# Performance work log

Hardware: AMD Instinct MI355X
Metric: run time of the kernel (lower is better)

Reference implementation:

```python
import jax, jax.numpy as jnp
import numpy as np

WINDOW_SIZE = 2
SOFTMAX_TEMP = 0.01


def get_indices(batch_size, window_size):
    # For each window, match keypoints of frame j against dense map of frame j+1.
    kp_inds, dense_inds = [], []
    for i in range(batch_size):
        for j in range(window_size - 1):
            idx = i * window_size + j
            kp_inds.append(idx)
            dense_inds.append(idx + 1)
    return np.array(kp_inds), np.array(dense_inds)


def l2_normalize(x, axis):
    n = jnp.sqrt(jnp.sum(x * x, axis=axis, keepdims=True))
    return x / jnp.maximum(n, 1e-12)


def grid_sample_bilinear(img, grid_u, grid_v):
    """torch.nn.functional.grid_sample, mode='bilinear', padding='zeros', align_corners=False.
    img: (B,C,H,W); grid_u, grid_v: (B,N) normalized coords in [-1,1]. Returns (B,C,N)."""
    B, C, H, W = img.shape
    x = ((grid_u + 1.0) * W - 1.0) * 0.5  # pixel x
    y = ((grid_v + 1.0) * H - 1.0) * 0.5  # pixel y
    x0 = jnp.floor(x)
    y0 = jnp.floor(y)
    wx1 = x - x0
    wy1 = y - y0
    flat = img.reshape(B, C, H * W)

    def gather(xi, yi):
        valid = (xi >= 0) & (xi <= W - 1) & (yi >= 0) & (yi <= H - 1)
        xi_c = jnp.clip(xi, 0, W - 1).astype(jnp.int32)
        yi_c = jnp.clip(yi, 0, H - 1).astype(jnp.int32)
        idx = yi_c * W + xi_c  # (B,N)
        vals = jnp.take_along_axis(flat, idx[:, None, :], axis=2)  # (B,C,N)
        return vals * valid[:, None, :].astype(img.dtype)

    out = (gather(x0, y0) * ((1 - wx1) * (1 - wy1))[:, None, :]
           + gather(x0 + 1, y0) * (wx1 * (1 - wy1))[:, None, :]
           + gather(x0, y0 + 1) * ((1 - wx1) * wy1)[:, None, :]
           + gather(x0 + 1, y0 + 1) * (wx1 * wy1)[:, None, :])
    return out


def setup_inputs() -> dict:
    key = jax.random.key(0)
    k1, k2, k3, k4 = jax.random.split(key, 4)
    BW, C, N, H, W = 8, 128, 512, 256, 256
    return {
        "keypoint_scores": jax.random.uniform(k1, (BW, 1, N), dtype=jnp.float32),
        "keypoint_desc": jax.random.normal(k2, (BW, C, N), dtype=jnp.float32),
        "scores_dense": jax.random.uniform(k3, (BW, 1, H, W), dtype=jnp.float32),
        "desc_dense": jax.random.normal(k4, (BW, C, H, W), dtype=jnp.float32),
    }


def reference(keypoint_scores, keypoint_desc, scores_dense, desc_dense):
    BW, C, N = keypoint_desc.shape
    batch_size = BW // WINDOW_SIZE
    _, _, H, W = desc_dense.shape
    kp_inds, dense_inds = get_indices(batch_size, WINDOW_SIZE)

    src_desc = l2_normalize(keypoint_desc[kp_inds], axis=1)  # (B,C,N)
    B = src_desc.shape[0]
    tgt_desc_dense = desc_dense[dense_inds]  # (B,C,H,W)
    tgt_unrolled = l2_normalize(tgt_desc_dense.reshape(B, C, H * W), axis=1)

    # cosine similarity scores (B,N,H*W) -> temperature softmax over dense map
    match_vals = jnp.einsum('bcn,bcm->bnm', src_desc, tgt_unrolled)
    soft_match_vals = jax.nn.softmax(match_vals / SOFTMAX_TEMP, axis=2)

    # soft-argmax: expected (u,v) pixel coordinates
    v_coord, u_coord = jnp.meshgrid(jnp.arange(H), jnp.arange(W), indexing='ij')
    coords = jnp.stack([u_coord.reshape(-1), v_coord.reshape(-1)], axis=1).astype(jnp.float32)  # (HW,2)
    pseudo_coords = jnp.einsum('bnm,mk->bnk', soft_match_vals, coords)  # (B,N,2)

    u_norm = 2.0 * pseudo_coords[:, :, 0] / (W - 1) - 1.0
    v_norm = 2.0 * pseudo_coords[:, :, 1] / (H - 1) - 1.0

    tgt_scores_dense = scores_dense[dense_inds]
    pseudo_scores = grid_sample_bilinear(tgt_scores_dense, u_norm, v_norm)  # (B,1,N)
    pseudo_desc = grid_sample_bilinear(tgt_desc_dense, u_norm, v_norm)      # (B,C,N)

    desc_match_score = jnp.sum(src_desc * pseudo_desc, axis=1, keepdims=True) / float(C)
    src_scores = keypoint_scores[kp_inds]
    match_weights = 0.5 * (desc_match_score + 1.0) * src_scores * pseudo_scores
    return (pseudo_coords, match_weights, soft_match_vals)
```

## Files before the change

### kernel.cpp

```cpp
#include <hip/hip_runtime.h>


typedef short  v8s __attribute__((ext_vector_type(8)));
typedef unsigned short v8u __attribute__((ext_vector_type(8)));
typedef float  v4f __attribute__((ext_vector_type(4)));

#define EXP2_SCALE 144.269504088896f
#define WAITV(N) asm volatile("s_waitcnt vmcnt(" #N ")" ::: "memory")
#define SBAR()   __builtin_amdgcn_s_barrier()
#define SCHED()  __builtin_amdgcn_sched_barrier(0)
#define PRIO(N)  __builtin_amdgcn_s_setprio(N)

static const size_t O_AHI  = 0;
static const size_t O_ALO  = O_AHI  + 262144ull*2;
static const size_t O_SRCN = O_ALO  + 262144ull*2;
static const size_t O_BHI  = O_SRCN + 262144ull*4;
static const size_t O_BLO  = O_BHI  + 33554432ull*2;
static const size_t O_PART = O_BLO  + 33554432ull*2;
static const size_t O_ROWS = O_PART + 2048ull*64*16;

static __device__ inline unsigned short f2bf(float x) {
    unsigned u = __float_as_uint(x);
    u = u + 0x7FFFu + ((u >> 16) & 1u);
    return (unsigned short)(u >> 16);
}
static __device__ inline float bf2f(unsigned short h) {
    return __uint_as_float(((unsigned)h) << 16);
}

__device__ __forceinline__ void gl_lds16(const void* g, void* l) {
    auto gp = (const __attribute__((address_space(1))) unsigned int*)(uintptr_t)g;
    auto lp = (__attribute__((address_space(3))) unsigned int*)(uintptr_t)l;
    __builtin_amdgcn_global_load_lds(gp, lp, 16, 0, 0);
}

__global__ void __launch_bounds__(256) k_prep_src(const float* __restrict__ kd,
                                                  float* __restrict__ srcN,
                                                  unsigned short* __restrict__ Ahi,
                                                  unsigned short* __restrict__ Alo) {
    int gw = blockIdx.x * 4 + (threadIdx.x >> 6);
    int l  = threadIdx.x & 63;
    int b  = gw >> 9, n = gw & 511;
    const float* base = kd + (size_t)(2 * b) * 128 * 512;
    float x0 = base[l * 512 + n];
    float x1 = base[(l + 64) * 512 + n];
    float ss = x0 * x0 + x1 * x1;
#pragma unroll
    for (int m = 1; m < 64; m <<= 1) ss += __shfl_xor(ss, m, 64);
    float inv = 1.0f / fmaxf(sqrtf(ss), 1e-12f);
    float xn0 = x0 * inv, xn1 = x1 * inv;
    int ob = gw * 128;
    srcN[ob + l] = xn0;  srcN[ob + l + 64] = xn1;
    unsigned short h0 = f2bf(xn0), h1 = f2bf(xn1);
    Ahi[ob + l] = h0;        Ahi[ob + l + 64] = h1;
    Alo[ob + l] = f2bf(xn0 - bf2f(h0));
    Alo[ob + l + 64] = f2bf(xn1 - bf2f(h1));
}

__global__ void __launch_bounds__(256) k_prep_tgt(const float* __restrict__ dd,
                                                  unsigned short* __restrict__ Bhi,
                                                  unsigned short* __restrict__ Blo) {
    int t = blockIdx.x * 128 + (threadIdx.x >> 1);
    int h = threadIdx.x & 1;
    int b = t >> 16;
    int p = t & 65535;
    const float* src = dd + (size_t)(2 * b + 1) * 128 * 65536 + (size_t)(h * 64) * 65536 + p;
    float v[64];
    float ss = 0.f;
#pragma unroll
    for (int c = 0; c < 64; ++c) { float x = src[(size_t)c * 65536]; v[c] = x; ss += x * x; }
    ss += __shfl_xor(ss, 1, 64);
    float inv = 1.0f / fmaxf(sqrtf(ss), 1e-12f);
    size_t ob = (size_t)t * 128 + h * 64;
#pragma unroll
    for (int c8 = 0; c8 < 8; ++c8) {
        v8u h8, l8;
#pragma unroll
        for (int j = 0; j < 8; ++j) {
            float xn = v[c8 * 8 + j] * inv;
            unsigned short hh = f2bf(xn);
            h8[j] = hh;
            l8[j] = f2bf(xn - bf2f(hh));
        }
        *(v8u*)(Bhi + ob + c8 * 8) = h8;
        *(v8u*)(Blo + ob + c8 * 8) = l8;
    }
}

template <int MODE>
__global__ void __launch_bounds__(512, 2) k_gemm(const unsigned short* __restrict__ Ahi,
                                                 const unsigned short* __restrict__ Alo,
                                                 const unsigned short* __restrict__ Bhi,
                                                 const unsigned short* __restrict__ Blo,
                                                 const float4* __restrict__ rows,
                                                 float* __restrict__ part,
                                                 float* __restrict__ out,
                                                 const float* __restrict__ ksc,
                                                 const float* __restrict__ sd,
                                                 const float* __restrict__ dd,
                                                 const float* __restrict__ srcN) {
    __shared__ v4f bstage4[8192];
    char* bstage = (char*)bstage4;

    const int tid = threadIdx.x;
    const int l = tid & 63, w = tid >> 6;
    const int wm = w >> 2, wn = w & 3;
    const int l15 = l & 15, l16 = l >> 4;
    const int mtg = blockIdx.x, ny = blockIdx.y, b = blockIdx.z;
    const int mt0 = mtg * 16;
    float* osm = out + 6144;

    v8s ahi[2][4], alo[2][4];
    {
        const size_t ar = ((size_t)(b * 512 + ny * 128 + wn * 32 + l15)) * 128 + l16 * 8;
#pragma unroll
        for (int nf = 0; nf < 2; ++nf)
#pragma unroll
            for (int ksl = 0; ksl < 4; ++ksl) {
                ahi[nf][ksl] = *(const v8s*)(Ahi + ar + nf * 2048 + ksl * 32);
                alo[nf][ksl] = *(const v8s*)(Alo + ar + nf * 2048 + ksl * 32);
            }
    }
    float invs[2];
    if (MODE == 1) {
#pragma unroll
        for (int nf = 0; nf < 2; ++nf)
            invs[nf] = rows[b * 512 + ny * 128 + wn * 32 + nf * 16 + l15].x;
    }
    WAITV(0);

    const size_t pxbase = ((size_t)b * 65536 + (size_t)mt0 * 128) * 128;

#define STAGEU(SRC, eoff, bufidx)                                                   \
    {                                                                               \
        const unsigned short* src_ = (SRC) + pxbase + (eoff);                       \
        char* dst_ = bstage + (bufidx) * 32768;                                     \
        _Pragma("unroll")                                                           \
        for (int i = 0; i < 4; ++i) {                                               \
            int sl = tid + i * 512;                                                 \
            int rl = sl >> 4, gg = sl & 15;                                         \
            gl_lds16(src_ + rl * 128 + ((gg ^ (rl & 15)) << 3), dst_ + (sl << 4));  \
        }                                                                           \
    }
#define PXF(bufbase, mf_, ksl_)                                                     \
    (*(const v8s*)((bufbase) + (wm * 64 + (mf_) * 16 + l15) * 256 +                 \
                   ((((ksl_) * 4 + l16) ^ ((wm * 64 + (mf_) * 16 + l15) & 15)) << 4)))

    v4f acc[4][2];

    if (MODE == 0) {
        float sS[2] = {0.f, 0.f}, sU[2] = {0.f, 0.f}, sV[2] = {0.f, 0.f};
        STAGEU(Bhi, 0, 0);
        STAGEU(Bhi, 16384, 1);
#pragma unroll 1
        for (int mt = 0; mt < 16; ++mt) {
            if (mt == 15) WAITV(0); else WAITV(4);
            SBAR(); SCHED();
            if (mt < 14) STAGEU(Bhi, (size_t)(mt + 2) * 16384, (mt + 2) & 3);
            const char* bb = bstage + (mt & 3) * 32768;
#pragma unroll
            for (int mf = 0; mf < 4; ++mf)
#pragma unroll
                for (int nf = 0; nf < 2; ++nf) { v4f z = {0.f,0.f,0.f,0.f}; acc[mf][nf] = z; }
            PRIO(1);
#pragma unroll
            for (int ksl = 0; ksl < 4; ++ksl) {
                v8s pxf[4];
#pragma unroll
                for (int mf = 0; mf < 4; ++mf) pxf[mf] = PXF(bb, mf, ksl);
#pragma unroll
                for (int mf = 0; mf < 4; ++mf)
#pragma unroll
                    for (int nf = 0; nf < 2; ++nf) {
                        acc[mf][nf] = __builtin_amdgcn_mfma_f32_16x16x32_bf16(pxf[mf], ahi[nf][ksl], acc[mf][nf], 0, 0, 0);
                        acc[mf][nf] = __builtin_amdgcn_mfma_f32_16x16x32_bf16(pxf[mf], alo[nf][ksl], acc[mf][nf], 0, 0, 0);
                    }
            }
            PRIO(0);
            SCHED();
            const int mtv = mt0 + mt;
            float ts[2] = {0.f, 0.f};
#pragma unroll
            for (int mf = 0; mf < 4; ++mf) {
                int mloc = wm * 64 + mf * 16 + l16 * 4;
#pragma unroll
                for (int nf = 0; nf < 2; ++nf)
#pragma unroll
                    for (int r = 0; r < 4; ++r) {
                        float e = __builtin_amdgcn_exp2f(fmaf(acc[mf][nf][r], EXP2_SCALE, -EXP2_SCALE));
                        ts[nf] += e;
                        sU[nf] = fmaf(e, (float)(mloc + r), sU[nf]);
                    }
            }
#pragma unroll
            for (int nf = 0; nf < 2; ++nf) {
                sS[nf] += ts[nf];
                sV[nf] = fmaf(ts[nf], (float)(mtv >> 1), sV[nf]);
                if (mtv & 1) sU[nf] = fmaf(ts[nf], 128.f, sU[nf]);
            }
        }
#pragma unroll
        for (int nf = 0; nf < 2; ++nf) {
            sS[nf] += __shfl_xor(sS[nf], 16, 64); sS[nf] += __shfl_xor(sS[nf], 32, 64);
            sU[nf] += __shfl_xor(sU[nf], 16, 64); sU[nf] += __shfl_xor(sU[nf], 32, 64);
            sV[nf] += __shfl_xor(sV[nf], 16, 64); sV[nf] += __shfl_xor(sV[nf], 32, 64);
        }
        if (l < 16) {
#pragma unroll
            for (int nf = 0; nf < 2; ++nf) {
                int row = b * 512 + ny * 128 + wn * 32 + nf * 16 + l15;
                ((float4*)part)[((size_t)row * 32 + mtg) * 2 + wm]
                    = make_float4(sS[nf], sU[nf], sV[nf], 0.f);
            }
        }
    } else {
        STAGEU(Bhi, 0, 0);
        STAGEU(Blo, 0, 1);
#pragma unroll 1
        for (int ph = 0; ph < 32; ++ph) {
            if (ph <= 1) WAITV(4);
            else if (ph == 31) WAITV(8);
            else WAITV(12);
            SBAR(); SCHED();
            if (ph < 30) {
                const int pn = ph + 2;
                const size_t eoff = (size_t)(pn >> 1) * 16384;
                if ((pn & 1) == 0) STAGEU(Bhi, eoff, pn & 3)
                else               STAGEU(Blo, eoff, pn & 3)
            }
            const char* bb = bstage + (ph & 3) * 32768;
            const int sub = ph & 1;
            if (sub == 0) {
#pragma unroll
                for (int mf = 0; mf < 4; ++mf)
#pragma unroll
                    for (int nf = 0; nf < 2; ++nf) { v4f z = {0.f,0.f,0.f,0.f}; acc[mf][nf] = z; }
            }
            PRIO(1);
#pragma unroll
            for (int ksl = 0; ksl < 4; ++ksl) {
                v8s pxf[4];
#pragma unroll
                for (int mf = 0; mf < 4; ++mf) pxf[mf] = PXF(bb, mf, ksl);
#pragma unroll
                for (int mf = 0; mf < 4; ++mf)
#pragma unroll
                    for (int nf = 0; nf < 2; ++nf) {
                        acc[mf][nf] = __builtin_amdgcn_mfma_f32_16x16x32_bf16(pxf[mf], ahi[nf][ksl], acc[mf][nf], 0, 0, 0);
                        if (sub == 0)
                            acc[mf][nf] = __builtin_amdgcn_mfma_f32_16x16x32_bf16(pxf[mf], alo[nf][ksl], acc[mf][nf], 0, 0, 0);
                    }
            }
            PRIO(0);
            SCHED();
            if (sub == 1) {
                int mt = ph >> 1;
                size_t mg0 = (size_t)(mt0 + mt) * 128 + wm * 64 + l16 * 4;
#pragma unroll
                for (int mf = 0; mf < 4; ++mf)
#pragma unroll
                    for (int nf = 0; nf < 2; ++nf) {
                        v4f pv;
#pragma unroll
                        for (int r = 0; r < 4; ++r)
                            pv[r] = __builtin_amdgcn_exp2f(fmaf(acc[mf][nf][r], EXP2_SCALE, -EXP2_SCALE)) * invs[nf];
                        size_t ng = (size_t)(b * 512 + ny * 128 + wn * 32 + nf * 16 + l15);
                        __builtin_nontemporal_store(pv, (v4f*)(osm + ng * 65536 + mg0 + mf * 16));
                    }
            }
        }

        if (w < 4) {
            const int bidx = mtg + 32 * ny + 128 * b;
            const int r = bidx * 4 + w;
            const int rb = r >> 9;
            float4 rs = rows[r];
            float u = rs.y, v = rs.z;
            float un = 2.0f * u / 255.0f - 1.0f;
            float vn = 2.0f * v / 255.0f - 1.0f;
            float x = ((un + 1.0f) * 256.0f - 1.0f) * 0.5f;
            float y = ((vn + 1.0f) * 256.0f - 1.0f) * 0.5f;
            float x0f = floorf(x), y0f = floorf(y);
            int x0 = (int)x0f, y0 = (int)y0f;
            int x1 = x0 + 1, y1 = y0 + 1;
            float wx1 = x - x0f, wy1 = y - y0f;
            float wx0 = 1.0f - wx1, wy0 = 1.0f - wy1;
            float m00 = ((x0 >= 0) & (x0 <= 255) & (y0 >= 0) & (y0 <= 255)) ? 1.f : 0.f;
            float m10 = ((x1 >= 0) & (x1 <= 255) & (y0 >= 0) & (y0 <= 255)) ? 1.f : 0.f;
            float m01 = ((x0 >= 0) & (x0 <= 255) & (y1 >= 0) & (y1 <= 255)) ? 1.f : 0.f;
            float m11 = ((x1 >= 0) & (x1 <= 255) & (y1 >= 0) & (y1 <= 255)) ? 1.f : 0.f;
            int cx0 = min(max(x0, 0), 255), cx1 = min(max(x1, 0), 255);
            int cy0 = min(max(y0, 0), 255), cy1 = min(max(y1, 0), 255);
            int i00 = cy0 * 256 + cx0, i10 = cy0 * 256 + cx1;
            int i01 = cy1 * 256 + cx0, i11 = cy1 * 256 + cx1;
            float w00 = wx0 * wy0 * m00, w10 = wx1 * wy0 * m10;
            float w01 = wx0 * wy1 * m01, w11 = wx1 * wy1 * m11;

            const float* sdb = sd + (size_t)(2 * rb + 1) * 65536;
            float ps = w00 * sdb[i00] + w10 * sdb[i10] + w01 * sdb[i01] + w11 * sdb[i11];

            const float* ddb = dd + (size_t)(2 * rb + 1) * 128 * 65536;
            float dot = 0.f;
#pragma unroll
            for (int h2 = 0; h2 < 2; ++h2) {
                int c = l + h2 * 64;
                const float* dc = ddb + (size_t)c * 65536;
                float pd = w00 * dc[i00] + w10 * dc[i10] + w01 * dc[i01] + w11 * dc[i11];
                dot += srcN[r * 128 + c] * pd;
            }
#pragma unroll
            for (int m = 1; m < 64; m <<= 1) dot += __shfl_xor(dot, m, 64);
            if (l == 0) {
                float dms = dot / 128.0f;
                float sscore = ksc[(2 * rb) * 512 + (r & 511)];
                out[4096 + r] = 0.5f * (dms + 1.0f) * sscore * ps;
            }
        }
    }
#undef STAGEU
#undef PXF
}

__global__ void __launch_bounds__(256) k_reduce(const float4* __restrict__ part,
                                                float4* __restrict__ rows,
                                                float* __restrict__ out) {
    int r = blockIdx.x * 4 + (threadIdx.x >> 6);
    int l = threadIdx.x & 63;
    float4 pp = part[(size_t)r * 64 + l];
    float S = pp.x, Su = pp.y, Sv = pp.z;
#pragma unroll
    for (int m = 1; m < 64; m <<= 1) {
        S += __shfl_xor(S, m, 64);
        Su += __shfl_xor(Su, m, 64);
        Sv += __shfl_xor(Sv, m, 64);
    }
    if (l == 0) {
        float invS = 1.0f / S;
        float u = Su * invS, v = Sv * invS;
        rows[r] = make_float4(invS, u, v, 0.f);
        out[r * 2] = u;
        out[r * 2 + 1] = v;
    }
}

extern "C" void kernel_launch(void* const* d_in, const int* in_sizes, int n_in,
                              void* d_out, int out_size, void* d_ws, size_t ws_size,
                              hipStream_t stream) {
    const float* ksc = (const float*)d_in[0];
    const float* kd  = (const float*)d_in[1];
    const float* sd  = (const float*)d_in[2];
    const float* dd  = (const float*)d_in[3];
    float* out = (float*)d_out;
    char* ws = (char*)d_ws;

    unsigned short* Ahi  = (unsigned short*)(ws + O_AHI);
    unsigned short* Alo  = (unsigned short*)(ws + O_ALO);
    float*          srcN = (float*)(ws + O_SRCN);
    unsigned short* Bhi  = (unsigned short*)(ws + O_BHI);
    unsigned short* Blo  = (unsigned short*)(ws + O_BLO);
    float*          part = (float*)(ws + O_PART);
    float4*         rows = (float4*)(ws + O_ROWS);

    k_prep_src<<<512, 256, 0, stream>>>(kd, srcN, Ahi, Alo);
    k_prep_tgt<<<2048, 256, 0, stream>>>(dd, Bhi, Blo);
    k_gemm<0><<<dim3(32, 4, 4), 512, 0, stream>>>(Ahi, Alo, Bhi, Blo, rows, part, out, ksc, sd, dd, srcN);
    k_reduce<<<512, 256, 0, stream>>>((const float4*)part, rows, out);
    k_gemm<1><<<dim3(32, 4, 4), 512, 0, stream>>>(Ahi, Alo, Bhi, Blo, rows, part, out, ksc, sd, dd, srcN);
}
```

Baseline: 387.1 us.

## Load Blo fragments directly to registers instead of staging through LDS

The second-pass loop now runs one iteration per M-tile instead of two phases. Only Bhi is staged into shared memory, while the Blo fragments are read straight from global memory into registers at the start of each iteration. The intent is to halve LDS staging traffic and the number of barriers, so all three MFMA products for a tile run back to back. The cost is more vector registers, the extra pxl array, and exposed global-load latency, which needs deeper vmcnt waits.

```diff
diff --git a/kernel.cpp b/kernel.cpp
--- a/kernel.cpp
+++ b/kernel.cpp
@@ -215,27 +215,31 @@
         }
     } else {
         STAGEU(Bhi, 0, 0);
-        STAGEU(Blo, 0, 1);
+        STAGEU(Bhi, 16384, 1);
 #pragma unroll 1
-        for (int ph = 0; ph < 32; ++ph) {
-            if (ph <= 1) WAITV(4);
-            else if (ph == 31) WAITV(8);
-            else WAITV(12);
+        for (int mt = 0; mt < 16; ++mt) {
+            if (mt == 0) WAITV(4);
+            else if (mt == 1) WAITV(28);
+            else if (mt == 15) WAITV(32);
+            else WAITV(36);
             SBAR(); SCHED();
-            if (ph < 30) {
-                const int pn = ph + 2;
-                const size_t eoff = (size_t)(pn >> 1) * 16384;
-                if ((pn & 1) == 0) STAGEU(Bhi, eoff, pn & 3)
-                else               STAGEU(Blo, eoff, pn & 3)
-            }
-            const char* bb = bstage + (ph & 3) * 32768;
-            const int sub = ph & 1;
-            if (sub == 0) {
+            v8s pxl[16];
+            {
+                const unsigned short* blo = Blo + pxbase + (size_t)mt * 16384;
 #pragma unroll
                 for (int mf = 0; mf < 4; ++mf)
 #pragma unroll
-                    for (int nf = 0; nf < 2; ++nf) { v4f z = {0.f,0.f,0.f,0.f}; acc[mf][nf] = z; }
-            }
+                    for (int ksl = 0; ksl < 4; ++ksl)
+                        pxl[mf * 4 + ksl] = *(const v8s*)(blo + (wm * 64 + mf * 16 + l15) * 128 + ksl * 32 + l16 * 8);
+            }
+            SCHED();
+            if (mt < 14) STAGEU(Bhi, (size_t)(mt + 2) * 16384, (mt + 2) & 3);
+            SCHED();
+            const char* bb = bstage + (mt & 3) * 32768;
+#pragma unroll
+            for (int mf = 0; mf < 4; ++mf)
+#pragma unroll
+                for (int nf = 0; nf < 2; ++nf) { v4f z = {0.f,0.f,0.f,0.f}; acc[mf][nf] = z; }
             PRIO(1);
 #pragma unroll
             for (int ksl = 0; ksl < 4; ++ksl) {
@@ -247,27 +251,31 @@
 #pragma unroll
                     for (int nf = 0; nf < 2; ++nf) {
                         acc[mf][nf] = __builtin_amdgcn_mfma_f32_16x16x32_bf16(pxf[mf], ahi[nf][ksl], acc[mf][nf], 0, 0, 0);
-                        if (sub == 0)
-                            acc[mf][nf] = __builtin_amdgcn_mfma_f32_16x16x32_bf16(pxf[mf], alo[nf][ksl], acc[mf][nf], 0, 0, 0);
+                        acc[mf][nf] = __builtin_amdgcn_mfma_f32_16x16x32_bf16(pxf[mf], alo[nf][ksl], acc[mf][nf], 0, 0, 0);
                     }
             }
+            SCHED();
+#pragma unroll
+            for (int ksl = 0; ksl < 4; ++ksl)
+#pragma unroll
+                for (int mf = 0; mf < 4; ++mf)
+#pragma unroll
+                    for (int nf = 0; nf < 2; ++nf)
+                        acc[mf][nf] = __builtin_amdgcn_mfma_f32_16x16x32_bf16(pxl[mf * 4 + ksl], ahi[nf][ksl], acc[mf][nf], 0, 0, 0);
             PRIO(0);
             SCHED();
-            if (sub == 1) {
-                int mt = ph >> 1;
-                size_t mg0 = (size_t)(mt0 + mt) * 128 + wm * 64 + l16 * 4;
-#pragma unroll
-                for (int mf = 0; mf < 4; ++mf)
-#pragma unroll
-                    for (int nf = 0; nf < 2; ++nf) {
-                        v4f pv;
-#pragma unroll
-                        for (int r = 0; r < 4; ++r)
-                            pv[r] = __builtin_amdgcn_exp2f(fmaf(acc[mf][nf][r], EXP2_SCALE, -EXP2_SCALE)) * invs[nf];
-                        size_t ng = (size_t)(b * 512 + ny * 128 + wn * 32 + nf * 16 + l15);
-                        __builtin_nontemporal_store(pv, (v4f*)(osm + ng * 65536 + mg0 + mf * 16));
-                    }
-            }
+            size_t mg0 = (size_t)(mt0 + mt) * 128 + wm * 64 + l16 * 4;
+#pragma unroll
+            for (int mf = 0; mf < 4; ++mf)
+#pragma unroll
+                for (int nf = 0; nf < 2; ++nf) {
+                    v4f pv;
+#pragma unroll
+                    for (int r = 0; r < 4; ++r)
+                        pv[r] = __builtin_amdgcn_exp2f(fmaf(acc[mf][nf][r], EXP2_SCALE, -EXP2_SCALE)) * invs[nf];
+                    size_t ng = (size_t)(b * 512 + ny * 128 + wn * 32 + nf * 16 + l15);
+                    __builtin_nontemporal_store(pv, (v4f*)(osm + ng * 65536 + mg0 + mf * 16));
+                }
         }
 
         if (w < 4) {
```

Measured after the change: 393.5 us. Within noise of the previous version (+1.6%).
